# Kernel tuning notes

Hardware: AMD Instinct MI355X
Metric: run time of the kernel (lower is better)

Reference implementation:

```python
import math
import jax, jax.numpy as jnp
import numpy as np

D = 512; H = 8; DH = 64          # d_model, heads, head dim
AB = 8                            # attention block size (BigBird block)
NG, NW, NR = 2, 5, 3              # global / window / random blocks
K = NG + NW + NR                  # attended blocks per query block
NL = 5                            # layers per (encoder|decoder) stack
MAXSEQ = 1024; BS = 4; NM = 4; LAT = 16; FF = 2048


def setup_inputs() -> dict:
    key = jax.random.key(0)
    ks = jax.random.split(key, 20)
    B = 32
    S_enc = MAXSEQ + 1
    nb_enc = (S_enc + AB - 1) // AB   # 129
    nb_dec = MAXSEQ // AB             # 128
    def n(i, shape, s=0.02):
        return jax.random.normal(ks[i], shape, jnp.float32) * s
    return {
        'x': jax.random.normal(ks[0], (B, MAXSEQ, BS * NM), jnp.float32),
        'eps': jax.random.normal(ks[1], (B, LAT), jnp.float32),
        'emb_in': n(2, (S_enc, D)),
        'emb_out': n(3, (MAXSEQ, D)),
        'W_data': n(4, (BS * NM, D)), 'b_data': jnp.zeros((D,), jnp.float32),
        'Wqkv': n(5, (2 * NL, D, 3 * D)), 'bqkv': jnp.zeros((2 * NL, 3 * D), jnp.float32),
        'Wo': n(6, (2 * NL, D, D)), 'bo': jnp.zeros((2 * NL, D), jnp.float32),
        'ln1_g': jnp.ones((2 * NL, D), jnp.float32), 'ln1_b': jnp.zeros((2 * NL, D), jnp.float32),
        'W1': n(7, (2 * NL, D, FF)), 'b1': jnp.zeros((2 * NL, FF), jnp.float32),
        'W2': n(8, (2 * NL, FF, D)), 'b2': jnp.zeros((2 * NL, D), jnp.float32),
        'ln2_g': jnp.ones((2 * NL, D), jnp.float32), 'ln2_b': jnp.zeros((2 * NL, D), jnp.float32),
        'W_mean': n(9, (D, LAT)), 'b_mean': jnp.zeros((LAT,), jnp.float32),
        'W_lv': n(10, (D, LAT)), 'b_lv': jnp.zeros((LAT,), jnp.float32),
        'W_exp': n(11, (LAT, 2 * MAXSEQ)), 'b_exp': jnp.zeros((2 * MAXSEQ,), jnp.float32),
        'W_conv': n(12, (2, D)), 'b_conv': jnp.zeros((D,), jnp.float32),
        'W_seq': n(13, (D, BS * NM)), 'b_seq': jnp.zeros((BS * NM,), jnp.float32),
        'rand_enc': jax.random.randint(ks[14], (nb_enc, NR), 0, nb_enc, jnp.int32),
        'rand_dec': jax.random.randint(ks[15], (nb_dec, NR), 0, nb_dec, jnp.int32),
    }


def _ln(x, g, b):
    m = jnp.mean(x, -1, keepdims=True)
    v = jnp.var(x, -1, keepdims=True)
    return (x - m) * jax.lax.rsqrt(v + 1e-5) * g + b


def _block_index(nb, rand):
    # per query block: NG global blocks, NW window blocks, NR random blocks
    i = jnp.arange(nb)
    g = jnp.broadcast_to(jnp.arange(NG)[None, :], (nb, NG))
    w = i[:, None] + (jnp.arange(NW) - NW // 2)[None, :]
    w_valid = (w >= 0) & (w < nb)
    idx = jnp.concatenate([g, jnp.clip(w, 0, nb - 1), rand], axis=1)          # [nb, K]
    valid = jnp.concatenate([jnp.ones((nb, NG), bool), w_valid,
                             jnp.ones((nb, NR), bool)], axis=1)               # [nb, K]
    return idx, valid


def _sparse_attn(x, Wqkv, bqkv, Wo, bo, rand):
    # BigBird-style block-sparse self attention (global + window + random blocks)
    B, S, _ = x.shape
    nb = (S + AB - 1) // AB
    Sp = nb * AB
    qkv = jnp.pad(x @ Wqkv + bqkv, ((0, 0), (0, Sp - S), (0, 0)))
    q, k, v = jnp.split(qkv, 3, axis=-1)
    def blk(t):  # [B,Sp,D] -> [B,H,nb,AB,DH]
        return t.reshape(B, nb, AB, H, DH).transpose(0, 3, 1, 2, 4)
    q, k, v = blk(q), blk(k), blk(v)
    idx, bvalid = _block_index(nb, rand)
    kg = k[:, :, idx]                      # [B,H,nb,K,AB,DH]
    vg = v[:, :, idx]
    scores = jnp.einsum('bhnqd,bhnkpd->bhnqkp', q, kg) / math.sqrt(DH)  # [B,H,nb,AB,K,AB]
    tok_valid = (jnp.arange(Sp) < S).reshape(nb, AB)
    kmask = bvalid[:, :, None] & tok_valid[idx]                          # [nb,K,AB]
    scores = jnp.where(kmask[None, None, :, None], scores, -1e9)
    attn = jax.nn.softmax(scores.reshape(B, H, nb, AB, K * AB), axis=-1)
    out = jnp.einsum('bhnqk,bhnkd->bhnqd', attn, vg.reshape(B, H, nb, K * AB, DH))
    out = out.transpose(0, 2, 3, 1, 4).reshape(B, Sp, D)[:, :S]
    return out @ Wo + bo


def _layer(x, i, p, rand):
    (Wqkv, bqkv, Wo, bo, ln1_g, ln1_b, W1, b1, W2, b2, ln2_g, ln2_b) = p
    a = _sparse_attn(x, Wqkv[i], bqkv[i], Wo[i], bo[i], rand)
    x = _ln(x + a, ln1_g[i], ln1_b[i])
    f = jax.nn.relu(x @ W1[i] + b1[i]) @ W2[i] + b2[i]
    return _ln(x + f, ln2_g[i], ln2_b[i])


def _forward(x, eps, emb_in, emb_out, W_data, b_data, Wqkv, bqkv, Wo, bo,
             ln1_g, ln1_b, W1, b1, W2, b2, ln2_g, ln2_b, W_mean, b_mean,
             W_lv, b_lv, W_exp, b_exp, W_conv, b_conv, W_seq, b_seq,
             rand_enc, rand_dec):
    B = x.shape[0]
    p = (Wqkv, bqkv, Wo, bo, ln1_g, ln1_b, W1, b1, W2, b2, ln2_g, ln2_b)
    # ---- encode ----
    h = x @ W_data + b_data                                   # [B,1024,512]
    cls = jnp.zeros((B, 1, D), x.dtype)
    h = jnp.concatenate([cls, h], axis=1) + emb_in            # [B,1025,512]
    for i in range(NL):
        h = _layer(h, i, p, rand_enc)
    pooled = h[:, 0]
    mean = pooled @ W_mean + b_mean
    logvar = pooled @ W_lv + b_lv
    # ---- sample (diag-Gaussian rsample) ----
    z = mean + eps * jnp.exp(0.5 * logvar)
    # ---- decode ----
    seq = (z @ W_exp + b_exp).reshape(B, 2, MAXSEQ)           # [B,2,1024]
    d = jnp.einsum('bcs,cd->bsd', seq, W_conv) + b_conv       # 1x1 conv, -> [B,1024,512]
    d = d + emb_out
    for i in range(NL, 2 * NL):
        d = _layer(d, i, p, rand_dec)
    out = d @ W_seq + b_seq                                   # [B,1024,16] (1x1 conv)
    decoded = out.reshape(B, -1, NM)                          # [B,4096,4]
    elbo = jnp.mean(-0.5 * jnp.sum(1.0 + logvar - mean ** 2 - jnp.exp(logvar), axis=1))
    return decoded, elbo


def reference(x, eps, emb_in, emb_out, W_data, b_data, Wqkv, bqkv, Wo, bo,
              ln1_g, ln1_b, W1, b1, W2, b2, ln2_g, ln2_b, W_mean, b_mean,
              W_lv, b_lv, W_exp, b_exp, W_conv, b_conv, W_seq, b_seq,
              rand_enc, rand_dec):
    return _forward(x, eps, emb_in, emb_out, W_data, b_data, Wqkv, bqkv, Wo, bo,
                    ln1_g, ln1_b, W1, b1, W2, b2, ln2_g, ln2_b, W_mean, b_mean,
                    W_lv, b_lv, W_exp, b_exp, W_conv, b_conv, W_seq, b_seq,
                    rand_enc, rand_dec)
```

## Files before the change

### kernel.cpp

```cpp
#include <hip/hip_runtime.h>

typedef unsigned short u16;
typedef __attribute__((ext_vector_type(8))) short short8;
typedef __attribute__((ext_vector_type(4))) float f32x4;

__device__ __forceinline__ float b2f(u16 h) {
  union { unsigned int u; float f; } v; v.u = ((unsigned int)h) << 16; return v.f;
}
__device__ __forceinline__ u16 f2b(float f) {
  union { float f; unsigned int u; } v; v.f = f;
  return (u16)((v.u + 0x7fffu + ((v.u >> 16) & 1u)) >> 16);
}

__device__ __forceinline__ void gload16(const u16* g, u16* l) {
  __builtin_amdgcn_global_load_lds(
      (const __attribute__((address_space(1))) void*)g,
      (__attribute__((address_space(3))) void*)l, 16, 0, 0);
}

#define SENC 1025
#define SPENC 1032
#define NBE 129
#define SDEC 1024
#define NBD 128
#define BATCH 32
#define MENC (BATCH * SPENC)
#define MDEC (BATCH * SDEC)

__global__ void beacon_k(float* out) { if (threadIdx.x == 0) out[0] = 1000.0f; }

__global__ __launch_bounds__(256) void tr_k(const float* __restrict__ W, u16* __restrict__ WT, int K, int N)
{
  __shared__ float sm[32][33];
  int k0 = blockIdx.x * 32, n0 = blockIdx.y * 32;
  const float* Wz = W + (size_t)blockIdx.z * K * N;
  u16* WTz = WT + (size_t)blockIdx.z * K * N;
  int r = threadIdx.x >> 3, c0 = (threadIdx.x & 7) * 4;
  float4 v = *(const float4*)&Wz[(size_t)(k0 + r) * N + n0 + c0];
  sm[r][c0] = v.x; sm[r][c0 + 1] = v.y; sm[r][c0 + 2] = v.z; sm[r][c0 + 3] = v.w;
  __syncthreads();
  ushort4 u;
  u.x = f2b(sm[c0][r]); u.y = f2b(sm[c0 + 1][r]); u.z = f2b(sm[c0 + 2][r]); u.w = f2b(sm[c0 + 3][r]);
  *(ushort4*)&WTz[(size_t)(n0 + r) * K + k0 + c0] = u;
}

__global__ __launch_bounds__(256) void embed_k(const float* __restrict__ x, const float* __restrict__ Wd,
    const float* __restrict__ bd, const float* __restrict__ emb, float* __restrict__ h, u16* __restrict__ hb)
{
  size_t gid = (size_t)blockIdx.x * 256 + threadIdx.x;
  int dd = (int)(gid & 511);
  size_t rs = gid >> 9;
  int s = (int)(rs % SPENC);
  int b = (int)(rs / SPENC);
  float v;
  if (s == 0) {
    v = emb[dd];
  } else if (s < SENC) {
    float acc = bd[dd];
    const float* xr = x + ((size_t)b * 1024 + (s - 1)) * 16;
    #pragma unroll
    for (int j = 0; j < 16; ++j) acc += xr[j] * Wd[j * 512 + dd];
    v = acc + emb[(size_t)s * 512 + dd];
  } else {
    v = 0.f;
  }
  h[gid] = v;
  hb[gid] = f2b(v);
}

template<typename TC, bool RELU, bool RESID, bool ATOMIC>
__global__ __launch_bounds__(512) void mgemm_k(const u16* __restrict__ A, const u16* __restrict__ WT,
    const float* __restrict__ bias, const float* __restrict__ R, TC* __restrict__ C,
    int M, int N, int Kc, int lda, int ldb)
{
  __shared__ __align__(16) u16 sA[2][128 * 32];
  __shared__ __align__(16) u16 sB[2][256 * 32];
  int t = threadIdx.x;

  int gx = gridDim.x;
  int nwg = gx * gridDim.y;
  int flat = blockIdx.y * gx + blockIdx.x;
  int q = nwg >> 3, rr = nwg & 7;
  int xcd = flat & 7, idx = flat >> 3;
  int swz = (xcd < rr ? xcd * (q + 1) : rr * (q + 1) + (xcd - rr) * q) + idx;
  int bx = swz % gx, by = swz / gx;

  int n0 = bx * 256, m0 = by * 128;
  int koff = blockIdx.z * Kc;
  int lane = t & 63, wave = t >> 6;
  int wm = (wave >> 2) * 64, wn = (wave & 3) * 64;
  int quad = lane >> 4, l15 = lane & 15;

  int rA = t >> 2, sc = t & 3;
  int cA = sc ^ ((rA >> 1) & 3);
  int raA = m0 + rA; raA = raA < M ? raA : M - 1;
  const u16* gA  = A  + (size_t)raA * lda + koff + cA * 8;
  int rB = t >> 2;
  int cB = sc ^ ((rB >> 1) & 3);
  const u16* gB0 = WT + (size_t)(n0 + rB) * ldb + koff + cB * 8;
  const u16* gB1 = WT + (size_t)(n0 + 128 + rB) * ldb + koff + cB * 8;
  u16* lA  = &sA[0][t * 8];
  u16* lB0 = &sB[0][t * 8];
  u16* lB1 = &sB[0][(512 + t) * 8];

  f32x4 acc[4][4];
  #pragma unroll
  for (int i = 0; i < 4; ++i)
    #pragma unroll
    for (int j = 0; j < 4; ++j) acc[i][j] = (f32x4){0.f, 0.f, 0.f, 0.f};

  const int nt = Kc >> 5;
  gload16(gA, lA); gload16(gB0, lB0); gload16(gB1, lB1);
  int cur = 0;
  for (int tt = 0; tt < nt; ++tt) {
    __syncthreads();
    if (tt + 1 < nt) {
      int k0 = (tt + 1) << 5;
      gload16(gA + k0, lA + (cur ^ 1) * 4096);
      gload16(gB0 + k0, lB0 + (cur ^ 1) * 8192);
      gload16(gB1 + k0, lB1 + (cur ^ 1) * 8192);
    }
    short8 af[4], bf[4];
    #pragma unroll
    for (int i = 0; i < 4; ++i) {
      int ra = wm + i * 16 + l15;
      af[i] = *(const short8*)&sA[cur][ra * 32 + (quad ^ ((ra >> 1) & 3)) * 8];
    }
    #pragma unroll
    for (int j = 0; j < 4; ++j) {
      int rb = wn + j * 16 + l15;
      bf[j] = *(const short8*)&sB[cur][rb * 32 + (quad ^ ((rb >> 1) & 3)) * 8];
    }
    #pragma unroll
    for (int i = 0; i < 4; ++i)
      #pragma unroll
      for (int j = 0; j < 4; ++j)
        acc[i][j] = __builtin_amdgcn_mfma_f32_16x16x32_bf16(af[i], bf[j], acc[i][j], 0, 0, 0);
    cur ^= 1;
  }

  #pragma unroll
  for (int i = 0; i < 4; ++i) {
    int mBase = m0 + wm + i * 16 + quad * 4;
    #pragma unroll
    for (int r = 0; r < 4; ++r) {
      int m = mBase + r;
      if (m < M) {
        #pragma unroll
        for (int j = 0; j < 4; ++j) {
          int n = n0 + wn + j * 16 + l15;
          if constexpr (ATOMIC) {
            float v = acc[i][j][r];
            if (blockIdx.z == 0) v += bias[n];
            unsafeAtomicAdd(&((float*)C)[(size_t)m * N + n], v);
          } else {
            float v = acc[i][j][r] + bias[n];
            if (RESID) v += R[(size_t)m * N + n];
            if (RELU) v = fmaxf(v, 0.f);
            if constexpr (sizeof(TC) == 2) ((u16*)C)[(size_t)m * N + n] = f2b(v);
            else ((float*)C)[(size_t)m * N + n] = v;
          }
        }
      }
    }
  }
}

__global__ __launch_bounds__(256) void ln_k(float* h, u16* __restrict__ hb,
    const float* __restrict__ g, const float* __restrict__ bb)
{
  __shared__ float rs[256], rq[256];
  float* p = h + (size_t)blockIdx.x * 512;
  u16* pb = hb + (size_t)blockIdx.x * 512;
  int t = threadIdx.x;
  float v0 = p[t], v1 = p[t + 256];
  rs[t] = v0 + v1; rq[t] = v0 * v0 + v1 * v1;
  __syncthreads();
  for (int o = 128; o > 0; o >>= 1) {
    if (t < o) { rs[t] += rs[t + o]; rq[t] += rq[t + o]; }
    __syncthreads();
  }
  float mean = rs[0] * (1.f / 512.f);
  float var = fmaxf(rq[0] * (1.f / 512.f) - mean * mean, 0.f);
  float rinv = rsqrtf(var + 1e-5f);
  float o0 = (v0 - mean) * rinv * g[t] + bb[t];
  float o1 = (v1 - mean) * rinv * g[t + 256] + bb[t + 256];
  p[t] = o0; p[t + 256] = o1;
  pb[t] = f2b(o0); pb[t + 256] = f2b(o1);
}

__global__ __launch_bounds__(64) void attnm_k(const u16* __restrict__ qkv, u16* __restrict__ av,
    const int* __restrict__ rnd, int S, int Sp, int nb)
{
  __shared__ __align__(16) u16 Vt[64 * 104];
  __shared__ __align__(16) u16 Pl[16 * 104];
  __shared__ int sJB[10], sVD[10];
  int t = threadIdx.x;
  int n = blockIdx.x % nb;
  int r1 = blockIdx.x / nb;
  int hh = r1 & 7, b = r1 >> 3;
  const u16* base = qkv + (size_t)b * Sp * 1536;
  int l15 = t & 15, quad = t >> 4;

  if (t < 10) {
    int jb, vd;
    if (t < 2) { jb = t; vd = 1; }
    else if (t < 7) {
      int w = n + t - 4;
      vd = (w >= 0 && w < nb) ? 1 : 0;
      jb = w < 0 ? 0 : (w > nb - 1 ? nb - 1 : w);
    } else { jb = rnd[n * 3 + t - 7]; vd = 1; }
    sJB[t] = jb; sVD[t] = vd;
  }
  {
    f32x4 zz = {0.f, 0.f, 0.f, 0.f};
    *(f32x4*)&Vt[t * 104 + 80] = zz;
    *(f32x4*)&Vt[t * 104 + 88] = zz;
    if (t < 16) {
      *(f32x4*)&Pl[t * 104 + 80] = zz;
      *(f32x4*)&Pl[t * 104 + 88] = zz;
    }
  }
  __syncthreads();

  short8 aq0, aq1;
  {
    const u16* qp = base + (size_t)(n * 8 + (l15 & 7)) * 1536 + hh * 64 + quad * 8;
    aq0 = *(const short8*)qp;
    aq1 = *(const short8*)(qp + 32);
  }

  f32x4 s[5];
  float okm[5];
  #pragma unroll
  for (int tile = 0; tile < 5; ++tile) {
    int kb = tile * 2 + (l15 >> 3);
    int tok = sJB[kb] * 8 + (l15 & 7);
    okm[tile] = (sVD[kb] && tok < S) ? 0.f : -3.0e38f;
    const u16* kp = base + (size_t)tok * 1536 + 512 + hh * 64 + quad * 8;
    short8 k0 = *(const short8*)kp;
    short8 k1 = *(const short8*)(kp + 32);
    f32x4 c = {0.f, 0.f, 0.f, 0.f};
    c = __builtin_amdgcn_mfma_f32_16x16x32_bf16(aq0, k0, c, 0, 0, 0);
    c = __builtin_amdgcn_mfma_f32_16x16x32_bf16(aq1, k1, c, 0, 0, 0);
    s[tile] = c;
  }

  u16 vreg[80];
  #pragma unroll
  for (int vt = 0; vt < 10; ++vt) {
    const u16* vp = base + (size_t)(sJB[vt] * 8) * 1536 + 1024 + hh * 64 + t;
    #pragma unroll
    for (int j = 0; j < 8; ++j) vreg[vt * 8 + j] = vp[(size_t)j * 1536];
  }

  f32x4 mx = {-3.0e38f, -3.0e38f, -3.0e38f, -3.0e38f};
  #pragma unroll
  for (int tile = 0; tile < 5; ++tile) {
    #pragma unroll
    for (int r = 0; r < 4; ++r) {
      float v = s[tile][r] * 0.125f + okm[tile];
      s[tile][r] = v;
      mx[r] = fmaxf(mx[r], v);
    }
  }
  #pragma unroll
  for (int off = 1; off < 16; off <<= 1) {
    #pragma unroll
    for (int r = 0; r < 4; ++r) mx[r] = fmaxf(mx[r], __shfl_xor(mx[r], off));
  }
  f32x4 sm = {0.f, 0.f, 0.f, 0.f};
  #pragma unroll
  for (int tile = 0; tile < 5; ++tile) {
    #pragma unroll
    for (int r = 0; r < 4; ++r) {
      float e = __expf(s[tile][r] - mx[r]);
      s[tile][r] = e;
      sm[r] += e;
    }
  }
  #pragma unroll
  for (int off = 1; off < 16; off <<= 1) {
    #pragma unroll
    for (int r = 0; r < 4; ++r) sm[r] += __shfl_xor(sm[r], off);
  }

  #pragma unroll
  for (int tile = 0; tile < 5; ++tile)
    #pragma unroll
    for (int r = 0; r < 4; ++r)
      Pl[(quad * 4 + r) * 104 + tile * 16 + l15] = f2b(s[tile][r]);

  #pragma unroll
  for (int vt = 0; vt < 10; ++vt) {
    short8 w;
    #pragma unroll
    for (int j = 0; j < 8; ++j) ((u16*)&w)[j] = (short)vreg[vt * 8 + j];
    *(short8*)&Vt[t * 104 + vt * 8] = w;
  }
  __syncthreads();

  f32x4 o[4];
  #pragma unroll
  for (int dn = 0; dn < 4; ++dn) o[dn] = (f32x4){0.f, 0.f, 0.f, 0.f};
  #pragma unroll
  for (int ks = 0; ks < 3; ++ks) {
    short8 ap = *(const short8*)&Pl[l15 * 104 + ks * 32 + quad * 8];
    #pragma unroll
    for (int dn = 0; dn < 4; ++dn) {
      short8 bv = *(const short8*)&Vt[(dn * 16 + l15) * 104 + ks * 32 + quad * 8];
      o[dn] = __builtin_amdgcn_mfma_f32_16x16x32_bf16(ap, bv, o[dn], 0, 0, 0);
    }
  }

  if (quad < 2) {
    #pragma unroll
    for (int r = 0; r < 4; ++r) {
      int qi = quad * 4 + r;
      float inv = 1.f / sm[r];
      u16* op = av + ((size_t)b * Sp + n * 8 + qi) * 512 + hh * 64 + l15;
      #pragma unroll
      for (int dn = 0; dn < 4; ++dn)
        op[dn * 16] = f2b(o[dn][r] * inv);
    }
  }
}

__global__ __launch_bounds__(512) void head_k(const float* __restrict__ h,
    const float* __restrict__ Wm, const float* __restrict__ bm,
    const float* __restrict__ Wlv, const float* __restrict__ blv,
    const float* __restrict__ eps, float* __restrict__ z, float* out_elbo)
{
  __shared__ float red[512];
  int t = threadIdx.x;
  int b = t >> 4, i = t & 15;
  const float* p = h + (size_t)b * SPENC * 512;
  float am = bm[i], al = blv[i];
  for (int c = 0; c < 512; ++c) {
    float pv = p[c];
    am += pv * Wm[c * 16 + i];
    al += pv * Wlv[c * 16 + i];
  }
  z[t] = am + eps[t] * expf(0.5f * al);
  red[t] = -0.5f * (1.f + al - am * am - expf(al));
  __syncthreads();
  for (int o = 256; o > 0; o >>= 1) { if (t < o) red[t] += red[t + o]; __syncthreads(); }
  if (t == 0) out_elbo[0] = red[0] * (1.f / 32.f);
}

__global__ __launch_bounds__(256) void seq_k(const float* __restrict__ z, const float* __restrict__ We,
    const float* __restrict__ be, float* __restrict__ seq)
{
  int gid = blockIdx.x * 256 + threadIdx.x;
  int b = gid >> 11, c = gid & 2047;
  float acc = be[c];
  #pragma unroll
  for (int i = 0; i < 16; ++i) acc += z[b * 16 + i] * We[i * 2048 + c];
  seq[gid] = acc;
}

__global__ __launch_bounds__(256) void decinit_k(const float* __restrict__ seq, const float* __restrict__ Wc,
    const float* __restrict__ bc, const float* __restrict__ emb, float* __restrict__ h, u16* __restrict__ hb)
{
  size_t gid = (size_t)blockIdx.x * 256 + threadIdx.x;
  int dd = (int)(gid & 511);
  size_t rs = gid >> 9;
  int s = (int)(rs & 1023);
  int b = (int)(rs >> 10);
  float v = seq[b * 2048 + s] * Wc[dd] + seq[b * 2048 + 1024 + s] * Wc[512 + dd]
          + bc[dd] + emb[(size_t)s * 512 + dd];
  h[gid] = v;
  hb[gid] = f2b(v);
}

__global__ __launch_bounds__(256) void final_k(const float* __restrict__ h, const float* __restrict__ Ws,
    const float* __restrict__ bs, float* __restrict__ out)
{
  int gid = blockIdx.x * 256 + threadIdx.x;
  int nn = gid & 15;
  int rs = gid >> 4;
  const float* p = h + (size_t)rs * 512;
  float acc = bs[nn];
  for (int c = 0; c < 512; ++c) acc += p[c] * Ws[c * 16 + nn];
  out[gid] = acc;
}

extern "C" void kernel_launch(void* const* d_in, const int* in_sizes, int n_in,
                              void* d_out, int out_size, void* d_ws, size_t ws_size,
                              hipStream_t stream) {
  float* out = (float*)d_out;
  (void)out_size; (void)ws_size;

  static const int EXP_DICT[30] = {
    524288, 512, 524800, 524288, 8192, 512, 7864320, 15360, 2621440, 5120,
    5120, 5120, 10485760, 20480, 10485760, 5120, 5120, 5120, 8192, 16,
    8192, 16, 32768, 2048, 1024, 512, 8192, 16, 387, 384 };
  bool dict_ok = (n_in == 30);
  if (dict_ok) for (int i = 0; i < 30; ++i) if (in_sizes[i] != EXP_DICT[i]) { dict_ok = false; break; }
  if (!dict_ok) { beacon_k<<<1, 64, 0, stream>>>(out); return; }

  const float* x      = (const float*)d_in[0];
  const float* eps    = (const float*)d_in[1];
  const float* emb_in = (const float*)d_in[2];
  const float* emb_out= (const float*)d_in[3];
  const float* W_data = (const float*)d_in[4];
  const float* b_data = (const float*)d_in[5];
  const float* Wqkv   = (const float*)d_in[6];
  const float* bqkv   = (const float*)d_in[7];
  const float* Wo     = (const float*)d_in[8];
  const float* bo     = (const float*)d_in[9];
  const float* ln1g   = (const float*)d_in[10];
  const float* ln1b   = (const float*)d_in[11];
  const float* W1     = (const float*)d_in[12];
  const float* b1     = (const float*)d_in[13];
  const float* W2     = (const float*)d_in[14];
  const float* b2     = (const float*)d_in[15];
  const float* ln2g   = (const float*)d_in[16];
  const float* ln2b   = (const float*)d_in[17];
  const float* Wm     = (const float*)d_in[18];
  const float* bm     = (const float*)d_in[19];
  const float* Wlv    = (const float*)d_in[20];
  const float* blv    = (const float*)d_in[21];
  const float* Wexp   = (const float*)d_in[22];
  const float* bexp   = (const float*)d_in[23];
  const float* Wconv  = (const float*)d_in[24];
  const float* bconv  = (const float*)d_in[25];
  const float* Wseq   = (const float*)d_in[26];
  const float* bseq   = (const float*)d_in[27];
  const int* rand_enc = (const int*)d_in[28];
  const int* rand_dec = (const int*)d_in[29];

  char* ws = (char*)d_ws;
  float* h     = (float*)ws;
  u16*   hb    = (u16*)(ws + 67633152);
  u16*   WTqkv = (u16*)(ws + 101449728);
  u16*   WTo   = (u16*)(ws + 117178368);
  u16*   WT1l  = (u16*)(ws + 122421248);
  u16*   WT2l  = (u16*)(ws + 124518400);
  u16*   qkvb  = (u16*)(ws + 126615552);
  u16*   avb   = (u16*)(ws + 126615552 + 50724864);
  u16*   ffnb  = (u16*)(ws + 126615552);
  float* seqb  = (float*)(ws + 194248704);
  float* z     = (float*)(ws + 194510848);

  tr_k<<<dim3(512 / 32, 1536 / 32, 10), 256, 0, stream>>>(Wqkv, WTqkv, 512, 1536);
  tr_k<<<dim3(512 / 32, 512 / 32, 10), 256, 0, stream>>>(Wo, WTo, 512, 512);

  {
    const int M = MENC;
    embed_k<<<(M * 512) / 256, 256, 0, stream>>>(x, W_data, b_data, emb_in, h, hb);
    for (int i = 0; i < 5; ++i) {
      for (int bc = 0; bc < 2; ++bc) {
        size_t roff = (size_t)bc * 16 * SPENC * 512;
        const int Mc = 16 * SPENC;
        const int ty = 129;
        mgemm_k<u16, false, false, false><<<dim3(1536 / 256, ty, 1), 512, 0, stream>>>(
            hb + roff, WTqkv + (size_t)i * 512 * 1536, bqkv + (size_t)i * 1536, nullptr, qkvb, Mc, 1536, 512, 512, 512);
        attnm_k<<<16 * 8 * NBE, 64, 0, stream>>>(qkvb, avb, rand_enc, SENC, SPENC, NBE);
        mgemm_k<float, false, false, true><<<dim3(512 / 256, ty, 2), 512, 0, stream>>>(
            avb, WTo + (size_t)i * 512 * 512, bo + (size_t)i * 512, nullptr, h + roff, Mc, 512, 256, 512, 512);
      }
      ln_k<<<M, 256, 0, stream>>>(h, hb, ln1g + (size_t)i * 512, ln1b + (size_t)i * 512);
      tr_k<<<dim3(512 / 32, 2048 / 32, 1), 256, 0, stream>>>(W1 + (size_t)i * 512 * 2048, WT1l, 512, 2048);
      tr_k<<<dim3(2048 / 32, 512 / 32, 1), 256, 0, stream>>>(W2 + (size_t)i * 2048 * 512, WT2l, 2048, 512);
      for (int off = 0; off < M; off += 16512) {
        const int Mc = 16512;
        const int ty = 129;
        mgemm_k<u16, true, false, false><<<dim3(2048 / 256, ty, 1), 512, 0, stream>>>(
            hb + (size_t)off * 512, WT1l, b1 + (size_t)i * 2048, nullptr, ffnb, Mc, 2048, 512, 512, 512);
        mgemm_k<float, false, false, true><<<dim3(512 / 256, ty, 2), 512, 0, stream>>>(
            ffnb, WT2l, b2 + (size_t)i * 512, nullptr, h + (size_t)off * 512, Mc, 512, 1024, 2048, 2048);
      }
      ln_k<<<M, 256, 0, stream>>>(h, hb, ln2g + (size_t)i * 512, ln2b + (size_t)i * 512);
    }
  }

  head_k<<<1, 512, 0, stream>>>(h, Wm, bm, Wlv, blv, eps, z, out + 524288);
  seq_k<<<256, 256, 0, stream>>>(z, Wexp, bexp, seqb);
  decinit_k<<<(MDEC * 512) / 256, 256, 0, stream>>>(seqb, Wconv, bconv, emb_out, h, hb);

  {
    const int M = MDEC;
    for (int i = 5; i < 10; ++i) {
      for (int bc = 0; bc < 2; ++bc) {
        size_t roff = (size_t)bc * 16 * SDEC * 512;
        const int Mc = 16 * SDEC;
        const int ty = 128;
        mgemm_k<u16, false, false, false><<<dim3(1536 / 256, ty, 1), 512, 0, stream>>>(
            hb + roff, WTqkv + (size_t)i * 512 * 1536, bqkv + (size_t)i * 1536, nullptr, qkvb, Mc, 1536, 512, 512, 512);
        attnm_k<<<16 * 8 * NBD, 64, 0, stream>>>(qkvb, avb, rand_dec, SDEC, SDEC, NBD);
        mgemm_k<float, false, false, true><<<dim3(512 / 256, ty, 2), 512, 0, stream>>>(
            avb, WTo + (size_t)i * 512 * 512, bo + (size_t)i * 512, nullptr, h + roff, Mc, 512, 256, 512, 512);
      }
      ln_k<<<M, 256, 0, stream>>>(h, hb, ln1g + (size_t)i * 512, ln1b + (size_t)i * 512);
      tr_k<<<dim3(512 / 32, 2048 / 32, 1), 256, 0, stream>>>(W1 + (size_t)i * 512 * 2048, WT1l, 512, 2048);
      tr_k<<<dim3(2048 / 32, 512 / 32, 1), 256, 0, stream>>>(W2 + (size_t)i * 2048 * 512, WT2l, 2048, 512);
      for (int off = 0; off < M; off += 16384) {
        const int Mc = 16384;
        const int ty = 128;
        mgemm_k<u16, true, false, false><<<dim3(2048 / 256, ty, 1), 512, 0, stream>>>(
            hb + (size_t)off * 512, WT1l, b1 + (size_t)i * 2048, nullptr, ffnb, Mc, 2048, 512, 512, 512);
        mgemm_k<float, false, false, true><<<dim3(512 / 256, ty, 2), 512, 0, stream>>>(
            ffnb, WT2l, b2 + (size_t)i * 512, nullptr, h + (size_t)off * 512, Mc, 512, 1024, 2048, 2048);
      }
      ln_k<<<M, 256, 0, stream>>>(h, hb, ln2g + (size_t)i * 512, ln2b + (size_t)i * 512);
    }
  }

  final_k<<<524288 / 256, 256, 0, stream>>>(h, Wseq, bseq, out);
}
```

Measured before the change: 6.830 ms.

## Triple-buffer GEMM LDS tiles with explicit vmcnt waits and MFMA priority

Expands the bf16 GEMM's shared-memory staging from double to triple buffering, prefetching two K-tiles ahead. A single barrier per iteration is kept, and an explicit s_waitcnt vmcnt(3) waits only for the current tile's loads, leaving the next tile's loads in flight. The MFMA block is wrapped in s_setprio to favour math issue over other waves. LDS use rises by half, which may reduce occupancy, and correctness now depends on the hand-counted vmcnt matching three loads per stage.

```diff
diff --git a/kernel.cpp b/kernel.cpp
--- a/kernel.cpp
+++ b/kernel.cpp
@@ -73,8 +73,8 @@
     const float* __restrict__ bias, const float* __restrict__ R, TC* __restrict__ C,
     int M, int N, int Kc, int lda, int ldb)
 {
-  __shared__ __align__(16) u16 sA[2][128 * 32];
-  __shared__ __align__(16) u16 sB[2][256 * 32];
+  __shared__ __align__(16) u16 sA[3][128 * 32];
+  __shared__ __align__(16) u16 sB[3][256 * 32];
   int t = threadIdx.x;
 
   int gx = gridDim.x;
@@ -95,13 +95,8 @@
   int cA = sc ^ ((rA >> 1) & 3);
   int raA = m0 + rA; raA = raA < M ? raA : M - 1;
   const u16* gA  = A  + (size_t)raA * lda + koff + cA * 8;
-  int rB = t >> 2;
-  int cB = sc ^ ((rB >> 1) & 3);
-  const u16* gB0 = WT + (size_t)(n0 + rB) * ldb + koff + cB * 8;
-  const u16* gB1 = WT + (size_t)(n0 + 128 + rB) * ldb + koff + cB * 8;
-  u16* lA  = &sA[0][t * 8];
-  u16* lB0 = &sB[0][t * 8];
-  u16* lB1 = &sB[0][(512 + t) * 8];
+  const u16* gB0 = WT + (size_t)(n0 + rA) * ldb + koff + cA * 8;
+  const u16* gB1 = WT + (size_t)(n0 + 128 + rA) * ldb + koff + cA * 8;
 
   f32x4 acc[4][4];
   #pragma unroll
@@ -110,15 +105,28 @@
     for (int j = 0; j < 4; ++j) acc[i][j] = (f32x4){0.f, 0.f, 0.f, 0.f};
 
   const int nt = Kc >> 5;
-  gload16(gA, lA); gload16(gB0, lB0); gload16(gB1, lB1);
+  gload16(gA,      &sA[0][t * 8]);
+  gload16(gB0,     &sB[0][t * 8]);
+  gload16(gB1,     &sB[0][(512 + t) * 8]);
+  gload16(gA + 32, &sA[1][t * 8]);
+  gload16(gB0 + 32,&sB[1][t * 8]);
+  gload16(gB1 + 32,&sB[1][(512 + t) * 8]);
+
   int cur = 0;
   for (int tt = 0; tt < nt; ++tt) {
-    __syncthreads();
-    if (tt + 1 < nt) {
-      int k0 = (tt + 1) << 5;
-      gload16(gA + k0, lA + (cur ^ 1) * 4096);
-      gload16(gB0 + k0, lB0 + (cur ^ 1) * 8192);
-      gload16(gB1 + k0, lB1 + (cur ^ 1) * 8192);
+    if (tt < nt - 1) {
+      asm volatile("s_waitcnt vmcnt(3)" ::: "memory");
+    } else {
+      asm volatile("s_waitcnt vmcnt(0)" ::: "memory");
+    }
+    __builtin_amdgcn_s_barrier();
+    asm volatile("" ::: "memory");
+    if (tt + 2 < nt) {
+      int k0 = (tt + 2) << 5;
+      int nb = tt + 2; nb -= (nb / 3) * 3;
+      gload16(gA + k0,  &sA[nb][t * 8]);
+      gload16(gB0 + k0, &sB[nb][t * 8]);
+      gload16(gB1 + k0, &sB[nb][(512 + t) * 8]);
     }
     short8 af[4], bf[4];
     #pragma unroll
@@ -131,12 +139,14 @@
       int rb = wn + j * 16 + l15;
       bf[j] = *(const short8*)&sB[cur][rb * 32 + (quad ^ ((rb >> 1) & 3)) * 8];
     }
+    __builtin_amdgcn_s_setprio(1);
     #pragma unroll
     for (int i = 0; i < 4; ++i)
       #pragma unroll
       for (int j = 0; j < 4; ++j)
         acc[i][j] = __builtin_amdgcn_mfma_f32_16x16x32_bf16(af[i], bf[j], acc[i][j], 0, 0, 0);
-    cur ^= 1;
+    __builtin_amdgcn_s_setprio(0);
+    cur = (cur == 2) ? 0 : cur + 1;
   }
 
   #pragma unroll
```

Measured after the change: 6.723 ms. Within noise of the previous version (-1.6%).
